# Performance work log

Hardware: AMD Instinct MI355X
Metric: run time of the kernel (lower is better)

Reference implementation:

```python
import jax, jax.numpy as jnp
import numpy as np

B, S, V = 1, 4096, 50265
D, H, DH, FF, L = 768, 12, 64, 3072, 12
W = 256  # one-sided window (longformer-base attention_window=512)
EPS = 1e-5
NEG = -1e9


def _ln(x, s, b):
    mu = jnp.mean(x, -1, keepdims=True)
    var = jnp.mean(jnp.square(x - mu), -1, keepdims=True)
    return (x - mu) * jax.lax.rsqrt(var + EPS) * s + b


def _sliding_attn(q, k, v, key_mask):
    # q,k,v: [B,H,S,DH]; key_mask: [B,S] (1 = attend). Banded attention |i-j| <= W.
    b, h, s, dh = q.shape
    c = W
    nc = s // c
    idx = jnp.arange(nc)[:, None] * c + jnp.arange(3 * c)[None, :]  # index into padded key axis
    kp = jnp.pad(k, ((0, 0), (0, 0), (c, c), (0, 0)))
    vp = jnp.pad(v, ((0, 0), (0, 0), (c, c), (0, 0)))
    k3 = kp[:, :, idx]  # [B,H,nc,3c,DH]
    v3 = vp[:, :, idx]
    qc = q.reshape(b, h, nc, c, dh)
    scores = jnp.einsum('bhncd,bhnmd->bhncm', qc, k3) * (1.0 / (dh ** 0.5))
    rel = jnp.arange(3 * c)[None, :] - c - jnp.arange(c)[:, None]  # key_pos - query_pos, [c,3c]
    band = jnp.abs(rel) <= W
    km = jnp.pad(key_mask.astype(bool), ((0, 0), (c, c)))[:, idx]  # [B,nc,3c]
    valid = band[None, None, None] & km[:, None, :, None, :]
    probs = jax.nn.softmax(jnp.where(valid, scores, NEG), axis=-1)
    out = jnp.einsum('bhncm,bhnmd->bhncd', probs, v3)
    return out.reshape(b, h, s, dh)


def _forward(input_ids, attention_mask, word_emb, pos_emb, emb_ln_s, emb_ln_b,
             Wq, bq, Wk, bk, Wv, bv, Wo, bo, ln1_s, ln1_b,
             W1, b1, W2, b2, ln2_s, ln2_b,
             h1w, h1b, h2w, h2b, h3w, h3b):
    b, s = input_ids.shape
    pos = jnp.arange(s) + 2  # roberta-style position offset (padding_idx=1)
    x = word_emb[input_ids] + pos_emb[pos][None]
    x = _ln(x, emb_ln_s, emb_ln_b)
    key_mask = attention_mask

    def block(xc, p):
        wq, bq_, wk, bk_, wv, bv_, wo, bo_, l1s, l1b, w1, b1_, w2, b2_, l2s, l2b = p
        q = (xc @ wq + bq_).reshape(b, s, H, DH).transpose(0, 2, 1, 3)
        k = (xc @ wk + bk_).reshape(b, s, H, DH).transpose(0, 2, 1, 3)
        v = (xc @ wv + bv_).reshape(b, s, H, DH).transpose(0, 2, 1, 3)
        a = _sliding_attn(q, k, v, key_mask).transpose(0, 2, 1, 3).reshape(b, s, D)
        xc = _ln(xc + a @ wo + bo_, l1s, l1b)
        hdd = jax.nn.gelu(xc @ w1 + b1_, approximate=False)
        xc = _ln(xc + hdd @ w2 + b2_, l2s, l2b)
        return xc, None

    x, _ = jax.lax.scan(block, x, (Wq, bq, Wk, bk, Wv, bv, Wo, bo,
                                   ln1_s, ln1_b, W1, b1, W2, b2, ln2_s, ln2_b))

    # gather hidden state at last occurrence of token id 2 (</s>) per row
    eq = (input_ids == 2).astype(jnp.int32)
    sep = s - 1 - jnp.argmax(eq[:, ::-1], axis=1)
    emb = x[jnp.arange(b), sep]  # [B, D]

    z = jax.nn.relu(emb @ h1w + h1b)
    z = jax.nn.relu(z @ h2w + h2b)
    return jnp.tanh(z @ h3w + h3b)  # [B, 1]


def setup_inputs() -> dict:
    key = jax.random.key(0)
    ks = jax.random.split(key, 24)
    sc = 0.02

    def n(k, shape):
        return jax.random.normal(k, shape, jnp.float32) * sc

    input_ids = jax.random.randint(ks[0], (B, S), 0, V)
    input_ids = input_ids.at[:, -1].set(2)  # guarantee a </s> token (id 2)
    attention_mask = jnp.ones((B, S), jnp.int32)
    return {
        'input_ids': input_ids,
        'attention_mask': attention_mask,
        'word_emb': n(ks[1], (V, D)),
        'pos_emb': n(ks[2], (S + 2, D)),
        'emb_ln_s': jnp.ones((D,), jnp.float32),
        'emb_ln_b': jnp.zeros((D,), jnp.float32),
        'Wq': n(ks[3], (L, D, D)), 'bq': jnp.zeros((L, D), jnp.float32),
        'Wk': n(ks[4], (L, D, D)), 'bk': jnp.zeros((L, D), jnp.float32),
        'Wv': n(ks[5], (L, D, D)), 'bv': jnp.zeros((L, D), jnp.float32),
        'Wo': n(ks[6], (L, D, D)), 'bo': jnp.zeros((L, D), jnp.float32),
        'ln1_s': jnp.ones((L, D), jnp.float32), 'ln1_b': jnp.zeros((L, D), jnp.float32),
        'W1': n(ks[7], (L, D, FF)), 'b1': jnp.zeros((L, FF), jnp.float32),
        'W2': n(ks[8], (L, FF, D)), 'b2': jnp.zeros((L, D), jnp.float32),
        'ln2_s': jnp.ones((L, D), jnp.float32), 'ln2_b': jnp.zeros((L, D), jnp.float32),
        'h1w': n(ks[9], (D, 512)), 'h1b': jnp.zeros((512,), jnp.float32),
        'h2w': n(ks[10], (512, 256)), 'h2b': jnp.zeros((256,), jnp.float32),
        'h3w': n(ks[11], (256, 1)), 'h3b': jnp.zeros((1,), jnp.float32),
    }


def reference(input_ids, attention_mask, word_emb, pos_emb, emb_ln_s, emb_ln_b,
              Wq, bq, Wk, bk, Wv, bv, Wo, bo, ln1_s, ln1_b,
              W1, b1, W2, b2, ln2_s, ln2_b,
              h1w, h1b, h2w, h2b, h3w, h3b):
    return _forward(input_ids, attention_mask, word_emb, pos_emb, emb_ln_s, emb_ln_b,
                    Wq, bq, Wk, bk, Wv, bv, Wo, bo, ln1_s, ln1_b,
                    W1, b1, W2, b2, ln2_s, ln2_b,
                    h1w, h1b, h2w, h2b, h3w, h3b)
```

## Files before the change

kernel.cpp:

```cpp
#include <hip/hip_runtime.h>
#include <math.h>

#define S_LEN 4096
#define DMODEL 768
#define NHEAD 12
#define DHEAD 64
#define FFDIM 3072
#define NLAYER 12
#define WIN 256
#define QKVN 2304

typedef __bf16 bf16x8 __attribute__((ext_vector_type(8)));
typedef unsigned short u16x8 __attribute__((ext_vector_type(8)));
typedef float f32x4 __attribute__((ext_vector_type(4)));

__device__ inline unsigned short f2bf(float f) {
    unsigned int u = __float_as_uint(f);
    u += 0x7fff + ((u >> 16) & 1);
    return (unsigned short)(u >> 16);
}

__device__ inline void gload16(const void* g, void* l) {
    __builtin_amdgcn_global_load_lds((const __attribute__((address_space(1))) void*)g,
                                     (__attribute__((address_space(3))) void*)l, 16, 0, 0);
}


__device__ inline void block_reduce2(float& sum, float& sq) {
    #pragma unroll
    for (int off = 32; off; off >>= 1) {
        sum += __shfl_xor(sum, off);
        sq  += __shfl_xor(sq, off);
    }
    __shared__ float red[8];
    int wid = threadIdx.x >> 6, lane = threadIdx.x & 63;
    if (lane == 0) { red[wid] = sum; red[wid + 4] = sq; }
    __syncthreads();
    sum = red[0] + red[1] + red[2] + red[3];
    sq  = red[4] + red[5] + red[6] + red[7];
    __syncthreads();
}

__global__ __launch_bounds__(256) void ln_kernel(const float* __restrict__ in,
                                                 const float* __restrict__ s,
                                                 const float* __restrict__ b,
                                                 float* __restrict__ out,
                                                 unsigned short* __restrict__ outb) {
    int row = blockIdx.x, tid = threadIdx.x;
    const float* p = in + (size_t)row * DMODEL;
    float v0 = p[tid], v1 = p[tid + 256], v2 = p[tid + 512];
    float sum = v0 + v1 + v2;
    float sq  = v0 * v0 + v1 * v1 + v2 * v2;
    block_reduce2(sum, sq);
    float mu = sum * (1.0f / DMODEL);
    float var = sq * (1.0f / DMODEL) - mu * mu;
    float rs = rsqrtf(var + 1e-5f);
    float* o = out + (size_t)row * DMODEL;
    unsigned short* ob = outb + (size_t)row * DMODEL;
    float r0 = (v0 - mu) * rs * s[tid]       + b[tid];
    float r1 = (v1 - mu) * rs * s[tid + 256] + b[tid + 256];
    float r2 = (v2 - mu) * rs * s[tid + 512] + b[tid + 512];
    o[tid] = r0; o[tid + 256] = r1; o[tid + 512] = r2;
    ob[tid] = f2bf(r0); ob[tid + 256] = f2bf(r1); ob[tid + 512] = f2bf(r2);
}

__global__ __launch_bounds__(256) void embed_ln_kernel(const int* __restrict__ ids,
                                                       const float* __restrict__ wemb,
                                                       const float* __restrict__ pemb,
                                                       const float* __restrict__ s,
                                                       const float* __restrict__ b,
                                                       float* __restrict__ out,
                                                       unsigned short* __restrict__ outb) {
    int row = blockIdx.x, tid = threadIdx.x;
    int id = ids[row];
    const float* wp = wemb + (size_t)id * DMODEL;
    const float* pp = pemb + (size_t)(row + 2) * DMODEL;
    float v0 = wp[tid] + pp[tid];
    float v1 = wp[tid + 256] + pp[tid + 256];
    float v2 = wp[tid + 512] + pp[tid + 512];
    float sum = v0 + v1 + v2;
    float sq  = v0 * v0 + v1 * v1 + v2 * v2;
    block_reduce2(sum, sq);
    float mu = sum * (1.0f / DMODEL);
    float var = sq * (1.0f / DMODEL) - mu * mu;
    float rs = rsqrtf(var + 1e-5f);
    float* o = out + (size_t)row * DMODEL;
    unsigned short* ob = outb + (size_t)row * DMODEL;
    float r0 = (v0 - mu) * rs * s[tid]       + b[tid];
    float r1 = (v1 - mu) * rs * s[tid + 256] + b[tid + 256];
    float r2 = (v2 - mu) * rs * s[tid + 512] + b[tid + 512];
    o[tid] = r0; o[tid + 256] = r1; o[tid + 512] = r2;
    ob[tid] = f2bf(r0); ob[tid + 256] = f2bf(r1); ob[tid + 512] = f2bf(r2);
}

__global__ __launch_bounds__(256) void transpose_all(const float* __restrict__ wq,
                                                     const float* __restrict__ wk,
                                                     const float* __restrict__ wv,
                                                     const float* __restrict__ wo,
                                                     const float* __restrict__ w1,
                                                     const float* __restrict__ w2,
                                                     unsigned short* __restrict__ dq,
                                                     unsigned short* __restrict__ dk,
                                                     unsigned short* __restrict__ dv,
                                                     unsigned short* __restrict__ dwo,
                                                     unsigned short* __restrict__ d1,
                                                     unsigned short* __restrict__ d2) {
    const int id = blockIdx.x;
    const float* src; unsigned short* dst; int C, R, bx, by;
    if (id < 2304) {
        const int m = id / 576, t2 = id % 576;
        src = (m == 0) ? wq : (m == 1) ? wk : (m == 2) ? wv : wo;
        dst = (m == 0) ? dq : (m == 1) ? dk : (m == 2) ? dv : dwo;
        R = 768; C = 768; bx = (t2 % 24) * 32; by = (t2 / 24) * 32;
    } else if (id < 4608) {
        const int t2 = id - 2304;
        src = w1; dst = d1; R = 768; C = 3072;
        bx = (t2 % 96) * 32; by = (t2 / 96) * 32;
    } else {
        const int t2 = id - 4608;
        src = w2; dst = d2; R = 3072; C = 768;
        bx = (t2 % 24) * 32; by = (t2 / 24) * 32;
    }
    __shared__ float tile[32][33];
    const int tx = threadIdx.x & 31, ty = threadIdx.x >> 5;
    #pragma unroll
    for (int k = 0; k < 4; ++k)
        tile[ty + k * 8][tx] = src[(size_t)(by + ty + k * 8) * C + bx + tx];
    __syncthreads();
    #pragma unroll
    for (int k = 0; k < 4; ++k)
        dst[(size_t)(bx + ty + k * 8) * R + by + tx] = f2bf(tile[tx][ty + k * 8]);
}

__global__ __launch_bounds__(256) void bias_concat(const float* __restrict__ bq,
                                                   const float* __restrict__ bk,
                                                   const float* __restrict__ bv,
                                                   float* __restrict__ out) {
    int l = blockIdx.x, t = threadIdx.x;
    for (int i = t; i < DMODEL; i += 256) {
        out[(size_t)l * QKVN + i]              = bq[(size_t)l * DMODEL + i];
        out[(size_t)l * QKVN + DMODEL + i]     = bk[(size_t)l * DMODEL + i];
        out[(size_t)l * QKVN + 2 * DMODEL + i] = bv[(size_t)l * DMODEL + i];
    }
}

template<int MODE, int BN>
__global__ __launch_bounds__(256) void mfma_gemm(const unsigned short* __restrict__ A,
                                                 const unsigned short* __restrict__ Bt,
                                                 const float* __restrict__ bias,
                                                 const float* __restrict__ res,
                                                 void* __restrict__ Cout,
                                                 int M, int N, int K) {
    constexpr int MR = (BN == 128) ? 4 : 2;
    __shared__ unsigned short As[128 * 64];
    __shared__ unsigned short Bs[BN * 64];
    const int tid = threadIdx.x;
    const int wv = tid >> 6, lane = tid & 63;
    const int bm = blockIdx.x * 128, bn = blockIdx.y * BN;
    const int wr = (BN == 128) ? (wv >> 1) * 64 : wv * 32;
    const int wc = (BN == 128) ? (wv & 1) * 64 : 0;
    const int l15 = lane & 15, g = lane >> 4;

    f32x4 acc[MR][4];
    #pragma unroll
    for (int m = 0; m < MR; ++m)
        #pragma unroll
        for (int n = 0; n < 4; ++n)
            #pragma unroll
            for (int e = 0; e < 4; ++e) acc[m][n][e] = 0.f;

    const int srow = tid >> 3;
    const int scol = (tid & 7) * 8;

    for (int k0 = 0; k0 < K; k0 += 64) {
        __syncthreads();
        #pragma unroll
        for (int c = 0; c < 4; ++c)
            gload16(A + (size_t)(bm + c * 32 + srow) * K + k0 + scol,
                    (char*)As + c * 4096 + wv * 1024);
        #pragma unroll
        for (int c = 0; c < BN / 32; ++c)
            gload16(Bt + (size_t)(bn + c * 32 + srow) * K + k0 + scol,
                    (char*)Bs + c * 4096 + wv * 1024);
        __syncthreads();
        #pragma unroll
        for (int kk = 0; kk < 2; ++kk) {
            bf16x8 af[MR], bfr[4];
            #pragma unroll
            for (int m = 0; m < MR; ++m)
                af[m] = *(const bf16x8*)(As + (wr + m * 16 + l15) * 64 + kk * 32 + g * 8);
            #pragma unroll
            for (int n = 0; n < 4; ++n)
                bfr[n] = *(const bf16x8*)(Bs + (wc + n * 16 + l15) * 64 + kk * 32 + g * 8);
            #pragma unroll
            for (int m = 0; m < MR; ++m)
                #pragma unroll
                for (int n = 0; n < 4; ++n)
                    acc[m][n] = __builtin_amdgcn_mfma_f32_16x16x32_bf16(af[m], bfr[n], acc[m][n], 0, 0, 0);
        }
    }

    #pragma unroll
    for (int m = 0; m < MR; ++m) {
        const int row0 = bm + wr + m * 16 + g * 4;
        #pragma unroll
        for (int n = 0; n < 4; ++n) {
            const int col = bn + wc + n * 16 + l15;
            const float bb = bias[col];
            #pragma unroll
            for (int r = 0; r < 4; ++r) {
                float v = acc[m][n][r] + bb;
                if (MODE == 0) {
                    v += res[(size_t)(row0 + r) * N + col];
                    ((float*)Cout)[(size_t)(row0 + r) * N + col] = v;
                } else if (MODE == 1) {
                    ((unsigned short*)Cout)[(size_t)(row0 + r) * N + col] = f2bf(v);
                } else {
                    float gv = 0.5f * v * (1.0f + erff(v * 0.70710678118654752f));
                    ((unsigned short*)Cout)[(size_t)(row0 + r) * N + col] = f2bf(gv);
                }
            }
        }
    }
}

__global__ __launch_bounds__(256) void attn_mfma(const unsigned short* __restrict__ qkv,
                                                 const int* __restrict__ msk,
                                                 unsigned short* __restrict__ aout) {
    __shared__ unsigned short Ks[64 * 64];
    __shared__ unsigned short Vt[64 * 64];
    __shared__ unsigned short Ps[4][16 * 64];
    const int tid = threadIdx.x;
    const int wv = tid >> 6, lane = tid & 63;
    const int l15 = lane & 15, g = lane >> 4;
    const int h = blockIdx.y;
    const int q0 = blockIdx.x * 64;

    const int qrow = q0 + wv * 16 + l15;
    bf16x8 qf[2];
    #pragma unroll
    for (int kk = 0; kk < 2; ++kk)
        qf[kk] = *(const bf16x8*)(qkv + (size_t)qrow * QKVN + h * 64 + kk * 32 + g * 8);

    f32x4 o[4];
    #pragma unroll
    for (int n = 0; n < 4; ++n)
        #pragma unroll
        for (int e = 0; e < 4; ++e) o[n][e] = 0.f;
    float mst[4] = {-3e38f, -3e38f, -3e38f, -3e38f};
    float lst[4] = {0.f, 0.f, 0.f, 0.f};

    const int srow = tid >> 3;
    const int scol = (tid & 7) * 8;
    const int xr  = (l15 & 7) << 3;

    for (int c = 0; c < 9; ++c) {
        const int kc = q0 - 256 + c * 64;
        __syncthreads();
        #pragma unroll
        for (int cc = 0; cc < 2; ++cc) {
            const int r = cc * 32 + srow;
            int krow = min(max(kc + r, 0), S_LEN - 1);
            gload16(qkv + (size_t)krow * QKVN + DMODEL + h * 64 + (scol ^ ((r & 7) << 3)),
                    (char*)Ks + cc * 4096 + wv * 1024);
        }
        #pragma unroll
        for (int cc = 0; cc < 2; ++cc) {
            const int r = cc * 32 + srow;
            int vrow = min(max(kc + r, 0), S_LEN - 1);
            u16x8 vvv = *(const u16x8*)(qkv + (size_t)vrow * QKVN + 2 * DMODEL + h * 64 + scol);
            const int xb = (scol >> 3) & 7;
            #pragma unroll
            for (int j = 0; j < 8; ++j)
                Vt[(scol + j) * 64 + (r ^ ((xb ^ j) << 3))] = vvv[j];
        }
        __syncthreads();

        f32x4 s[4];
        #pragma unroll
        for (int n = 0; n < 4; ++n)
            #pragma unroll
            for (int e = 0; e < 4; ++e) s[n][e] = 0.f;
        #pragma unroll
        for (int kk = 0; kk < 2; ++kk) {
            #pragma unroll
            for (int n = 0; n < 4; ++n) {
                bf16x8 kf = *(const bf16x8*)(Ks + (n * 16 + l15) * 64 + ((kk * 32 + g * 8) ^ xr));
                s[n] = __builtin_amdgcn_mfma_f32_16x16x32_bf16(qf[kk], kf, s[n], 0, 0, 0);
            }
        }

        float pv[4][4];
        const int qbase = q0 + wv * 16 + g * 4;
        #pragma unroll
        for (int n = 0; n < 4; ++n) {
            const int key = kc + n * 16 + l15;
            const bool kin = (key >= 0) && (key < S_LEN);
            const int mv = kin ? msk[key] : 0;
            #pragma unroll
            for (int r = 0; r < 4; ++r) {
                const int qa = qbase + r;
                const bool valid = (mv != 0) && (abs(key - qa) <= WIN);
                pv[n][r] = valid ? s[n][r] * 0.125f : -1e9f;
            }
        }
        float scold[4];
        #pragma unroll
        for (int r = 0; r < 4; ++r) {
            float mx = fmaxf(fmaxf(pv[0][r], pv[1][r]), fmaxf(pv[2][r], pv[3][r]));
            mx = fmaxf(mx, __shfl_xor(mx, 1));
            mx = fmaxf(mx, __shfl_xor(mx, 2));
            mx = fmaxf(mx, __shfl_xor(mx, 4));
            mx = fmaxf(mx, __shfl_xor(mx, 8));
            const float nm = fmaxf(mst[r], mx);
            scold[r] = expf(mst[r] - nm);
            float sum = 0.f;
            #pragma unroll
            for (int n = 0; n < 4; ++n) { pv[n][r] = expf(pv[n][r] - nm); sum += pv[n][r]; }
            sum += __shfl_xor(sum, 1); sum += __shfl_xor(sum, 2);
            sum += __shfl_xor(sum, 4); sum += __shfl_xor(sum, 8);
            lst[r] = lst[r] * scold[r] + sum;
            mst[r] = nm;
        }
        #pragma unroll
        for (int n = 0; n < 4; ++n)
            #pragma unroll
            for (int r = 0; r < 4; ++r)
                o[n][r] *= scold[r];

        #pragma unroll
        for (int n = 0; n < 4; ++n)
            #pragma unroll
            for (int r = 0; r < 4; ++r) {
                const int ql = g * 4 + r;
                Ps[wv][ql * 64 + ((n * 16 + l15) ^ ((ql & 7) << 3))] = f2bf(pv[n][r]);
            }

        #pragma unroll
        for (int kk = 0; kk < 2; ++kk) {
            bf16x8 pf = *(const bf16x8*)(Ps[wv] + l15 * 64 + ((kk * 32 + g * 8) ^ xr));
            #pragma unroll
            for (int nd = 0; nd < 4; ++nd) {
                const int d = nd * 16 + l15;
                const int xv = (((nd * 2 + (l15 >> 3)) & 7) ^ (l15 & 7)) << 3;
                bf16x8 vf = *(const bf16x8*)(Vt + d * 64 + ((kk * 32 + g * 8) ^ xv));
                o[nd] = __builtin_amdgcn_mfma_f32_16x16x32_bf16(pf, vf, o[nd], 0, 0, 0);
            }
        }
    }

    #pragma unroll
    for (int r = 0; r < 4; ++r) {
        const float inv = 1.0f / lst[r];
        const int qa = q0 + wv * 16 + g * 4 + r;
        #pragma unroll
        for (int nd = 0; nd < 4; ++nd)
            aout[(size_t)qa * DMODEL + h * 64 + nd * 16 + l15] = f2bf(o[nd][r] * inv);
    }
}

__global__ __launch_bounds__(256) void head1_kernel(const int* __restrict__ ids,
                                                    const float* __restrict__ x,
                                                    const float* __restrict__ w1,
                                                    const float* __restrict__ b1,
                                                    float* __restrict__ z1) {
    const int tid = threadIdx.x;
    __shared__ int sred[256];
    int loc = -1;
    for (int i = tid; i < S_LEN; i += 256)
        if (ids[i] == 2) loc = i;
    sred[tid] = loc;
    __syncthreads();
    for (int s2 = 128; s2; s2 >>= 1) {
        if (tid < s2) sred[tid] = max(sred[tid], sred[tid + s2]);
        __syncthreads();
    }
    const int sep = sred[0] < 0 ? (S_LEN - 1) : sred[0];

    __shared__ float emb[DMODEL];
    for (int d = tid; d < DMODEL; d += 256) emb[d] = x[(size_t)sep * DMODEL + d];
    __syncthreads();

    const int o = blockIdx.x * 64 + (tid & 63);
    const int chunk = tid >> 6;
    float s = 0.f;
    const int d0 = chunk * 192;
    for (int d = d0; d < d0 + 192; ++d)
        s += emb[d] * w1[(size_t)d * 512 + o];
    __shared__ float part[4][64];
    part[chunk][tid & 63] = s;
    __syncthreads();
    if (chunk == 0) {
        float v = part[0][tid] + part[1][tid] + part[2][tid] + part[3][tid] + b1[o];
        z1[o] = fmaxf(v, 0.f);
    }
}

__global__ __launch_bounds__(256) void head2_kernel(const float* __restrict__ z1,
                                                    const float* __restrict__ w2,
                                                    const float* __restrict__ b2,
                                                    const float* __restrict__ w3,
                                                    const float* __restrict__ b3,
                                                    float* __restrict__ out) {
    const int tid = threadIdx.x;
    __shared__ float z1s[512];
    for (int i = tid; i < 512; i += 256) z1s[i] = z1[i];
    __syncthreads();
    float s = b2[tid];
    for (int d = 0; d < 512; ++d) s += z1s[d] * w2[(size_t)d * 256 + tid];
    float z2 = fmaxf(s, 0.f);
    __shared__ float fred[256];
    fred[tid] = z2 * w3[tid];
    __syncthreads();
    for (int s2 = 128; s2; s2 >>= 1) {
        if (tid < s2) fred[tid] += fred[tid + s2];
        __syncthreads();
    }
    if (tid == 0) out[0] = tanhf(fred[0] + b3[0]);
}


extern "C" void kernel_launch(void* const* d_in, const int* in_sizes, int n_in,
                              void* d_out, int out_size, void* d_ws, size_t ws_size,
                              hipStream_t stream) {
    const int*   ids      = (const int*)d_in[0];
    const int*   amask    = (const int*)d_in[1];
    const float* word_emb = (const float*)d_in[2];
    const float* pos_emb  = (const float*)d_in[3];
    const float* emb_s    = (const float*)d_in[4];
    const float* emb_b    = (const float*)d_in[5];
    const float* Wq = (const float*)d_in[6];
    const float* bq = (const float*)d_in[7];
    const float* Wk = (const float*)d_in[8];
    const float* bk = (const float*)d_in[9];
    const float* Wv = (const float*)d_in[10];
    const float* bv = (const float*)d_in[11];
    const float* Wo = (const float*)d_in[12];
    const float* bo = (const float*)d_in[13];
    const float* l1s = (const float*)d_in[14];
    const float* l1b = (const float*)d_in[15];
    const float* W1 = (const float*)d_in[16];
    const float* b1 = (const float*)d_in[17];
    const float* W2 = (const float*)d_in[18];
    const float* b2 = (const float*)d_in[19];
    const float* l2s = (const float*)d_in[20];
    const float* l2b = (const float*)d_in[21];
    const float* h1w = (const float*)d_in[22];
    const float* h1b = (const float*)d_in[23];
    const float* h2w = (const float*)d_in[24];
    const float* h2b = (const float*)d_in[25];
    const float* h3w = (const float*)d_in[26];
    const float* h3b = (const float*)d_in[27];

    char* ws = (char*)d_ws;
    float* x          = (float*)(ws);
    float* t          = (float*)(ws + 12582912);
    unsigned short* xb   = (unsigned short*)(ws + 25165824);
    unsigned short* qkv  = (unsigned short*)(ws + 31457280);
    unsigned short* a    = (unsigned short*)(ws + 50331648);
    unsigned short* hb   = (unsigned short*)(ws + 56623104);
    unsigned short* WqkvT= (unsigned short*)(ws + 81788928);
    unsigned short* WoT  = (unsigned short*)(ws + 85327872);
    unsigned short* W1T  = (unsigned short*)(ws + 86507520);
    unsigned short* W2T  = (unsigned short*)(ws + 91226112);
    float* biascat       = (float*)(ws + 95944704);
    float* z1ws          = (float*)(ws + 96055296);

    bias_concat<<<NLAYER, 256, 0, stream>>>(bq, bk, bv, biascat);
    embed_ln_kernel<<<S_LEN, 256, 0, stream>>>(ids, word_emb, pos_emb, emb_s, emb_b, x, xb);

    const size_t dd = (size_t)DMODEL * DMODEL;
    const size_t df = (size_t)DMODEL * FFDIM;

    for (int l = 0; l < NLAYER; ++l) {
        transpose_all<<<6912, 256, 0, stream>>>(Wq + l * dd, Wk + l * dd, Wv + l * dd, Wo + l * dd,
                                                W1 + l * df, W2 + l * df,
                                                WqkvT, WqkvT + dd, WqkvT + 2 * dd, WoT, W1T, W2T);

        mfma_gemm<1, 128><<<dim3(32, 18), 256, 0, stream>>>(xb, WqkvT, biascat + (size_t)l * QKVN,
                                                            nullptr, qkv, S_LEN, QKVN, DMODEL);
        attn_mfma<<<dim3(S_LEN / 64, NHEAD), 256, 0, stream>>>(qkv, amask, a);

        mfma_gemm<0, 64><<<dim3(32, 12), 256, 0, stream>>>(a, WoT, bo + (size_t)l * DMODEL,
                                                           x, t, S_LEN, DMODEL, DMODEL);
        ln_kernel<<<S_LEN, 256, 0, stream>>>(t, l1s + (size_t)l * DMODEL, l1b + (size_t)l * DMODEL, x, xb);

        mfma_gemm<2, 128><<<dim3(32, 24), 256, 0, stream>>>(xb, W1T, b1 + (size_t)l * FFDIM,
                                                            nullptr, hb, S_LEN, FFDIM, DMODEL);
        mfma_gemm<0, 64><<<dim3(32, 12), 256, 0, stream>>>(hb, W2T, b2 + (size_t)l * DMODEL,
                                                           x, t, S_LEN, DMODEL, FFDIM);
        ln_kernel<<<S_LEN, 256, 0, stream>>>(t, l2s + (size_t)l * DMODEL, l2b + (size_t)l * DMODEL, x, xb);
    }

    head1_kernel<<<8, 256, 0, stream>>>(ids, x, h1w, h1b, z1ws);
    head2_kernel<<<1, 256, 0, stream>>>(z1ws, h2w, h2b, h3w, h3b, (float*)d_out);
}
```

Before: 2.747 ms.

## Batch all-layer weight transposes into one launch and widen attention query tile

The per-layer weight transpose/convert kernels are replaced by a single launch that converts all twelve layers' weights into a contiguous bf16 buffer before the layer loop. This cuts launch count and lets the conversion run as one large grid. The attention kernel now gives each wave 32 query rows instead of 16, so each K/V chunk loaded into shared memory serves twice as many queries. The cost is ten key chunks instead of nine, more registers per thread and half as many blocks, which lowers parallelism. The workspace grows to hold every layer's converted weights.

```diff
diff --git a/kernel.cpp b/kernel.cpp
--- a/kernel.cpp
+++ b/kernel.cpp
@@ -13,6 +13,10 @@
 typedef __bf16 bf16x8 __attribute__((ext_vector_type(8)));
 typedef unsigned short u16x8 __attribute__((ext_vector_type(8)));
 typedef float f32x4 __attribute__((ext_vector_type(4)));
+
+#define WDD 589824
+#define WDF 2359296
+#define WLAYER 7077888
 
 __device__ inline unsigned short f2bf(float f) {
     unsigned int u = __float_as_uint(f);
@@ -93,33 +97,30 @@
     ob[tid] = f2bf(r0); ob[tid + 256] = f2bf(r1); ob[tid + 512] = f2bf(r2);
 }
 
-__global__ __launch_bounds__(256) void transpose_all(const float* __restrict__ wq,
-                                                     const float* __restrict__ wk,
-                                                     const float* __restrict__ wv,
-                                                     const float* __restrict__ wo,
-                                                     const float* __restrict__ w1,
-                                                     const float* __restrict__ w2,
-                                                     unsigned short* __restrict__ dq,
-                                                     unsigned short* __restrict__ dk,
-                                                     unsigned short* __restrict__ dv,
-                                                     unsigned short* __restrict__ dwo,
-                                                     unsigned short* __restrict__ d1,
-                                                     unsigned short* __restrict__ d2) {
-    const int id = blockIdx.x;
+__global__ __launch_bounds__(256) void transpose_all(const float* __restrict__ Wq,
+                                                     const float* __restrict__ Wk,
+                                                     const float* __restrict__ Wv,
+                                                     const float* __restrict__ Wo,
+                                                     const float* __restrict__ W1,
+                                                     const float* __restrict__ W2,
+                                                     unsigned short* __restrict__ wall) {
+    const int l  = blockIdx.x / 6912;
+    const int id = blockIdx.x % 6912;
+    unsigned short* base = wall + (size_t)l * WLAYER;
     const float* src; unsigned short* dst; int C, R, bx, by;
     if (id < 2304) {
         const int m = id / 576, t2 = id % 576;
-        src = (m == 0) ? wq : (m == 1) ? wk : (m == 2) ? wv : wo;
-        dst = (m == 0) ? dq : (m == 1) ? dk : (m == 2) ? dv : dwo;
+        src = ((m == 0) ? Wq : (m == 1) ? Wk : (m == 2) ? Wv : Wo) + (size_t)l * WDD;
+        dst = base + (size_t)m * WDD;
         R = 768; C = 768; bx = (t2 % 24) * 32; by = (t2 / 24) * 32;
     } else if (id < 4608) {
         const int t2 = id - 2304;
-        src = w1; dst = d1; R = 768; C = 3072;
-        bx = (t2 % 96) * 32; by = (t2 / 96) * 32;
+        src = W1 + (size_t)l * WDF; dst = base + 4 * (size_t)WDD;
+        R = 768; C = 3072; bx = (t2 % 96) * 32; by = (t2 / 96) * 32;
     } else {
         const int t2 = id - 4608;
-        src = w2; dst = d2; R = 3072; C = 768;
-        bx = (t2 % 24) * 32; by = (t2 / 24) * 32;
+        src = W2 + (size_t)l * WDF; dst = base + 4 * (size_t)WDD + WDF;
+        R = 3072; C = 768; bx = (t2 % 24) * 32; by = (t2 / 24) * 32;
     }
     __shared__ float tile[32][33];
     const int tx = threadIdx.x & 31, ty = threadIdx.x >> 5;
@@ -229,32 +230,40 @@
                                                  unsigned short* __restrict__ aout) {
     __shared__ unsigned short Ks[64 * 64];
     __shared__ unsigned short Vt[64 * 64];
-    __shared__ unsigned short Ps[4][16 * 64];
+    __shared__ unsigned short Ps[4][32 * 64];
     const int tid = threadIdx.x;
     const int wv = tid >> 6, lane = tid & 63;
     const int l15 = lane & 15, g = lane >> 4;
     const int h = blockIdx.y;
-    const int q0 = blockIdx.x * 64;
-
-    const int qrow = q0 + wv * 16 + l15;
-    bf16x8 qf[2];
-    #pragma unroll
-    for (int kk = 0; kk < 2; ++kk)
-        qf[kk] = *(const bf16x8*)(qkv + (size_t)qrow * QKVN + h * 64 + kk * 32 + g * 8);
-
-    f32x4 o[4];
-    #pragma unroll
-    for (int n = 0; n < 4; ++n)
-        #pragma unroll
-        for (int e = 0; e < 4; ++e) o[n][e] = 0.f;
-    float mst[4] = {-3e38f, -3e38f, -3e38f, -3e38f};
-    float lst[4] = {0.f, 0.f, 0.f, 0.f};
+    const int q0 = blockIdx.x * 128;
+
+    bf16x8 qf[2][2];
+    #pragma unroll
+    for (int m = 0; m < 2; ++m) {
+        const int qrow = q0 + wv * 32 + m * 16 + l15;
+        #pragma unroll
+        for (int kk = 0; kk < 2; ++kk)
+            qf[m][kk] = *(const bf16x8*)(qkv + (size_t)qrow * QKVN + h * 64 + kk * 32 + g * 8);
+    }
+
+    f32x4 o[2][4];
+    #pragma unroll
+    for (int m = 0; m < 2; ++m)
+        #pragma unroll
+        for (int n = 0; n < 4; ++n)
+            #pragma unroll
+            for (int e = 0; e < 4; ++e) o[m][n][e] = 0.f;
+    float mst[2][4], lst[2][4];
+    #pragma unroll
+    for (int m = 0; m < 2; ++m)
+        #pragma unroll
+        for (int r = 0; r < 4; ++r) { mst[m][r] = -3e38f; lst[m][r] = 0.f; }
 
     const int srow = tid >> 3;
     const int scol = (tid & 7) * 8;
     const int xr  = (l15 & 7) << 3;
 
-    for (int c = 0; c < 9; ++c) {
+    for (int c = 0; c < 10; ++c) {
         const int kc = q0 - 256 + c * 64;
         __syncthreads();
         #pragma unroll
@@ -276,87 +285,104 @@
         }
         __syncthreads();
 
-        f32x4 s[4];
-        #pragma unroll
-        for (int n = 0; n < 4; ++n)
-            #pragma unroll
-            for (int e = 0; e < 4; ++e) s[n][e] = 0.f;
+        f32x4 s[2][4];
+        #pragma unroll
+        for (int m = 0; m < 2; ++m)
+            #pragma unroll
+            for (int n = 0; n < 4; ++n)
+                #pragma unroll
+                for (int e = 0; e < 4; ++e) s[m][n][e] = 0.f;
         #pragma unroll
         for (int kk = 0; kk < 2; ++kk) {
+            bf16x8 kf[4];
+            #pragma unroll
+            for (int n = 0; n < 4; ++n)
+                kf[n] = *(const bf16x8*)(Ks + (n * 16 + l15) * 64 + ((kk * 32 + g * 8) ^ xr));
+            #pragma unroll
+            for (int m = 0; m < 2; ++m)
+                #pragma unroll
+                for (int n = 0; n < 4; ++n)
+                    s[m][n] = __builtin_amdgcn_mfma_f32_16x16x32_bf16(qf[m][kk], kf[n], s[m][n], 0, 0, 0);
+        }
+
+        #pragma unroll
+        for (int m = 0; m < 2; ++m) {
+            float pv[4][4];
+            const int qbase = q0 + wv * 32 + m * 16 + g * 4;
             #pragma unroll
             for (int n = 0; n < 4; ++n) {
-                bf16x8 kf = *(const bf16x8*)(Ks + (n * 16 + l15) * 64 + ((kk * 32 + g * 8) ^ xr));
-                s[n] = __builtin_amdgcn_mfma_f32_16x16x32_bf16(qf[kk], kf, s[n], 0, 0, 0);
+                const int key = kc + n * 16 + l15;
+                const bool kin = (key >= 0) && (key < S_LEN);
+                const int mv = kin ? msk[key] : 0;
+                #pragma unroll
+                for (int r = 0; r < 4; ++r) {
+                    const int qa = qbase + r;
+                    const bool valid = (mv != 0) && (abs(key - qa) <= WIN);
+                    pv[n][r] = valid ? s[m][n][r] * 0.125f : -1e9f;
+                }
             }
-        }
-
-        float pv[4][4];
-        const int qbase = q0 + wv * 16 + g * 4;
-        #pragma unroll
-        for (int n = 0; n < 4; ++n) {
-            const int key = kc + n * 16 + l15;
-            const bool kin = (key >= 0) && (key < S_LEN);
-            const int mv = kin ? msk[key] : 0;
+            float scold[4];
             #pragma unroll
             for (int r = 0; r < 4; ++r) {
-                const int qa = qbase + r;
-                const bool valid = (mv != 0) && (abs(key - qa) <= WIN);
-                pv[n][r] = valid ? s[n][r] * 0.125f : -1e9f;
+                float mx = fmaxf(fmaxf(pv[0][r], pv[1][r]), fmaxf(pv[2][r], pv[3][r]));
+                mx = fmaxf(mx, __shfl_xor(mx, 1));
+                mx = fmaxf(mx, __shfl_xor(mx, 2));
+                mx = fmaxf(mx, __shfl_xor(mx, 4));
+                mx = fmaxf(mx, __shfl_xor(mx, 8));
+                const float nm = fmaxf(mst[m][r], mx);
+                scold[r] = expf(mst[m][r] - nm);
+                float sum = 0.f;
+                #pragma unroll
+                for (int n = 0; n < 4; ++n) { pv[n][r] = expf(pv[n][r] - nm); sum += pv[n][r]; }
+                sum += __shfl_xor(sum, 1); sum += __shfl_xor(sum, 2);
+                sum += __shfl_xor(sum, 4); sum += __shfl_xor(sum, 8);
+                lst[m][r] = lst[m][r] * scold[r] + sum;
+                mst[m][r] = nm;
             }
-        }
-        float scold[4];
-        #pragma unroll
-        for (int r = 0; r < 4; ++r) {
-            float mx = fmaxf(fmaxf(pv[0][r], pv[1][r]), fmaxf(pv[2][r], pv[3][r]));
-            mx = fmaxf(mx, __shfl_xor(mx, 1));
-            mx = fmaxf(mx, __shfl_xor(mx, 2));
-            mx = fmaxf(mx, __shfl_xor(mx, 4));
-            mx = fmaxf(mx, __shfl_xor(mx, 8));
-            const float nm = fmaxf(mst[r], mx);
-            scold[r] = expf(mst[r] - nm);
-            float sum = 0.f;
-            #pragma unroll
-            for (int n = 0; n < 4; ++n) { pv[n][r] = expf(pv[n][r] - nm); sum += pv[n][r]; }
-            sum += __shfl_xor(sum, 1); sum += __shfl_xor(sum, 2);
-            sum += __shfl_xor(sum, 4); sum += __shfl_xor(sum, 8);
-            lst[r] = lst[r] * scold[r] + sum;
-            mst[r] = nm;
-        }
-        #pragma unroll
-        for (int n = 0; n < 4; ++n)
-            #pragma unroll
-            for (int r = 0; r < 4; ++r)
-                o[n][r] *= scold[r];
-
-        #pragma unroll
-        for (int n = 0; n < 4; ++n)
-            #pragma unroll
-            for (int r = 0; r < 4; ++r) {
-                const int ql = g * 4 + r;
-                Ps[wv][ql * 64 + ((n * 16 + l15) ^ ((ql & 7) << 3))] = f2bf(pv[n][r]);
-            }
+            #pragma unroll
+            for (int n = 0; n < 4; ++n)
+                #pragma unroll
+                for (int r = 0; r < 4; ++r)
+                    o[m][n][r] *= scold[r];
+
+            #pragma unroll
+            for (int n = 0; n < 4; ++n)
+                #pragma unroll
+                for (int r = 0; r < 4; ++r) {
+                    const int ql = m * 16 + g * 4 + r;
+                    Ps[wv][ql * 64 + ((n * 16 + l15) ^ ((ql & 7) << 3))] = f2bf(pv[n][r]);
+                }
+        }
 
         #pragma unroll
         for (int kk = 0; kk < 2; ++kk) {
-            bf16x8 pf = *(const bf16x8*)(Ps[wv] + l15 * 64 + ((kk * 32 + g * 8) ^ xr));
+            bf16x8 vf[4];
             #pragma unroll
             for (int nd = 0; nd < 4; ++nd) {
                 const int d = nd * 16 + l15;
                 const int xv = (((nd * 2 + (l15 >> 3)) & 7) ^ (l15 & 7)) << 3;
-                bf16x8 vf = *(const bf16x8*)(Vt + d * 64 + ((kk * 32 + g * 8) ^ xv));
-                o[nd] = __builtin_amdgcn_mfma_f32_16x16x32_bf16(pf, vf, o[nd], 0, 0, 0);
+                vf[nd] = *(const bf16x8*)(Vt + d * 64 + ((kk * 32 + g * 8) ^ xv));
             }
-        }
-    }
-
-    #pragma unroll
-    for (int r = 0; r < 4; ++r) {
-        const float inv = 1.0f / lst[r];
-        const int qa = q0 + wv * 16 + g * 4 + r;
-        #pragma unroll
-        for (int nd = 0; nd < 4; ++nd)
-            aout[(size_t)qa * DMODEL + h * 64 + nd * 16 + l15] = f2bf(o[nd][r] * inv);
-    }
+            #pragma unroll
+            for (int m = 0; m < 2; ++m) {
+                bf16x8 pf = *(const bf16x8*)(Ps[wv] + (m * 16 + l15) * 64 + ((kk * 32 + g * 8) ^ xr));
+                #pragma unroll
+                for (int nd = 0; nd < 4; ++nd)
+                    o[m][nd] = __builtin_amdgcn_mfma_f32_16x16x32_bf16(pf, vf[nd], o[m][nd], 0, 0, 0);
+            }
+        }
+    }
+
+    #pragma unroll
+    for (int m = 0; m < 2; ++m)
+        #pragma unroll
+        for (int r = 0; r < 4; ++r) {
+            const float inv = 1.0f / lst[m][r];
+            const int qa = q0 + wv * 32 + m * 16 + g * 4 + r;
+            #pragma unroll
+            for (int nd = 0; nd < 4; ++nd)
+                aout[(size_t)qa * DMODEL + h * 64 + nd * 16 + l15] = f2bf(o[m][nd][r] * inv);
+        }
 }
 
 __global__ __launch_bounds__(256) void head1_kernel(const int* __restrict__ ids,
@@ -459,27 +485,23 @@
     unsigned short* qkv  = (unsigned short*)(ws + 31457280);
     unsigned short* a    = (unsigned short*)(ws + 50331648);
     unsigned short* hb   = (unsigned short*)(ws + 56623104);
-    unsigned short* WqkvT= (unsigned short*)(ws + 81788928);
-    unsigned short* WoT  = (unsigned short*)(ws + 85327872);
-    unsigned short* W1T  = (unsigned short*)(ws + 86507520);
-    unsigned short* W2T  = (unsigned short*)(ws + 91226112);
-    float* biascat       = (float*)(ws + 95944704);
-    float* z1ws          = (float*)(ws + 96055296);
+    float* biascat       = (float*)(ws + 81788928);
+    float* z1ws          = (float*)(ws + 81920000);
+    unsigned short* wall = (unsigned short*)(ws + 100663296);
 
     bias_concat<<<NLAYER, 256, 0, stream>>>(bq, bk, bv, biascat);
+    transpose_all<<<6912 * NLAYER, 256, 0, stream>>>(Wq, Wk, Wv, Wo, W1, W2, wall);
     embed_ln_kernel<<<S_LEN, 256, 0, stream>>>(ids, word_emb, pos_emb, emb_s, emb_b, x, xb);
 
-    const size_t dd = (size_t)DMODEL * DMODEL;
-    const size_t df = (size_t)DMODEL * FFDIM;
-
     for (int l = 0; l < NLAYER; ++l) {
-        transpose_all<<<6912, 256, 0, stream>>>(Wq + l * dd, Wk + l * dd, Wv + l * dd, Wo + l * dd,
-                                                W1 + l * df, W2 + l * df,
-                                                WqkvT, WqkvT + dd, WqkvT + 2 * dd, WoT, W1T, W2T);
+        const unsigned short* WqkvT = wall + (size_t)l * WLAYER;
+        const unsigned short* WoT   = WqkvT + 3 * (size_t)WDD;
+        const unsigned short* W1T   = WqkvT + 4 * (size_t)WDD;
+        const unsigned short* W2T   = WqkvT + 4 * (size_t)WDD + WDF;
 
         mfma_gemm<1, 128><<<dim3(32, 18), 256, 0, stream>>>(xb, WqkvT, biascat + (size_t)l * QKVN,
                                                             nullptr, qkv, S_LEN, QKVN, DMODEL);
-        attn_mfma<<<dim3(S_LEN / 64, NHEAD), 256, 0, stream>>>(qkv, amask, a);
+        attn_mfma<<<dim3(S_LEN / 128, NHEAD), 256, 0, stream>>>(qkv, amask, a);
 
         mfma_gemm<0, 64><<<dim3(32, 12), 256, 0, stream>>>(a, WoT, bo + (size_t)l * DMODEL,
                                                            x, t, S_LEN, DMODEL, DMODEL);
```

New measurement: 3.288 ms. 1.2x slower.

## Batch all-layer weight transposes into one launch, vectorize stores, templatize GEMM dims

Applied to the files above, without the earlier changes.

Replaces the twelve per-layer transpose launches with a single launch that converts every layer's weights into a persistent per-layer bf16 buffer before the layer loop. The transpose write path now packs two bf16 values into 32-bit stores, and the GEMM problem sizes become template parameters so the compiler sees them as constants. The goal is to cut launch count and serialization between the transpose and the GEMMs, and to make both the transposes and the GEMM loops cheaper. In exchange it needs a much larger workspace holding all transposed layers, and that buffer must fit within the allocated workspace.

```diff
diff --git a/kernel.cpp b/kernel.cpp
--- a/kernel.cpp
+++ b/kernel.cpp
@@ -13,6 +13,10 @@
 typedef __bf16 bf16x8 __attribute__((ext_vector_type(8)));
 typedef unsigned short u16x8 __attribute__((ext_vector_type(8)));
 typedef float f32x4 __attribute__((ext_vector_type(4)));
+
+#define WDD 589824
+#define WDF 2359296
+#define WLAYER 7077888
 
 __device__ inline unsigned short f2bf(float f) {
     unsigned int u = __float_as_uint(f);
@@ -93,33 +97,30 @@
     ob[tid] = f2bf(r0); ob[tid + 256] = f2bf(r1); ob[tid + 512] = f2bf(r2);
 }
 
-__global__ __launch_bounds__(256) void transpose_all(const float* __restrict__ wq,
-                                                     const float* __restrict__ wk,
-                                                     const float* __restrict__ wv,
-                                                     const float* __restrict__ wo,
-                                                     const float* __restrict__ w1,
-                                                     const float* __restrict__ w2,
-                                                     unsigned short* __restrict__ dq,
-                                                     unsigned short* __restrict__ dk,
-                                                     unsigned short* __restrict__ dv,
-                                                     unsigned short* __restrict__ dwo,
-                                                     unsigned short* __restrict__ d1,
-                                                     unsigned short* __restrict__ d2) {
-    const int id = blockIdx.x;
+__global__ __launch_bounds__(256) void transpose_all(const float* __restrict__ Wq,
+                                                     const float* __restrict__ Wk,
+                                                     const float* __restrict__ Wv,
+                                                     const float* __restrict__ Wo,
+                                                     const float* __restrict__ W1,
+                                                     const float* __restrict__ W2,
+                                                     unsigned short* __restrict__ wall) {
+    const int l  = blockIdx.x / 6912;
+    const int id = blockIdx.x % 6912;
+    unsigned short* base = wall + (size_t)l * WLAYER;
     const float* src; unsigned short* dst; int C, R, bx, by;
     if (id < 2304) {
         const int m = id / 576, t2 = id % 576;
-        src = (m == 0) ? wq : (m == 1) ? wk : (m == 2) ? wv : wo;
-        dst = (m == 0) ? dq : (m == 1) ? dk : (m == 2) ? dv : dwo;
+        src = ((m == 0) ? Wq : (m == 1) ? Wk : (m == 2) ? Wv : Wo) + (size_t)l * WDD;
+        dst = base + (size_t)m * WDD;
         R = 768; C = 768; bx = (t2 % 24) * 32; by = (t2 / 24) * 32;
     } else if (id < 4608) {
         const int t2 = id - 2304;
-        src = w1; dst = d1; R = 768; C = 3072;
-        bx = (t2 % 96) * 32; by = (t2 / 96) * 32;
+        src = W1 + (size_t)l * WDF; dst = base + 4 * (size_t)WDD;
+        R = 768; C = 3072; bx = (t2 % 96) * 32; by = (t2 / 96) * 32;
     } else {
         const int t2 = id - 4608;
-        src = w2; dst = d2; R = 3072; C = 768;
-        bx = (t2 % 24) * 32; by = (t2 / 24) * 32;
+        src = W2 + (size_t)l * WDF; dst = base + 4 * (size_t)WDD + WDF;
+        R = 3072; C = 768; bx = (t2 % 24) * 32; by = (t2 / 24) * 32;
     }
     __shared__ float tile[32][33];
     const int tx = threadIdx.x & 31, ty = threadIdx.x >> 5;
@@ -127,9 +128,15 @@
     for (int k = 0; k < 4; ++k)
         tile[ty + k * 8][tx] = src[(size_t)(by + ty + k * 8) * C + bx + tx];
     __syncthreads();
-    #pragma unroll
-    for (int k = 0; k < 4; ++k)
-        dst[(size_t)(bx + ty + k * 8) * R + by + tx] = f2bf(tile[tx][ty + k * 8]);
+    const int c16 = threadIdx.x >> 4;
+    const int rp  = threadIdx.x & 15;
+    #pragma unroll
+    for (int k = 0; k < 2; ++k) {
+        const int c = c16 + k * 16;
+        unsigned int lo = f2bf(tile[2 * rp][c]);
+        unsigned int hi = f2bf(tile[2 * rp + 1][c]);
+        *(unsigned int*)&dst[(size_t)(bx + c) * R + by + 2 * rp] = (hi << 16) | lo;
+    }
 }
 
 __global__ __launch_bounds__(256) void bias_concat(const float* __restrict__ bq,
@@ -144,13 +151,12 @@
     }
 }
 
-template<int MODE, int BN>
+template<int MODE, int BN, int M, int N, int K>
 __global__ __launch_bounds__(256) void mfma_gemm(const unsigned short* __restrict__ A,
                                                  const unsigned short* __restrict__ Bt,
                                                  const float* __restrict__ bias,
                                                  const float* __restrict__ res,
-                                                 void* __restrict__ Cout,
-                                                 int M, int N, int K) {
+                                                 void* __restrict__ Cout) {
     constexpr int MR = (BN == 128) ? 4 : 2;
     __shared__ unsigned short As[128 * 64];
     __shared__ unsigned short Bs[BN * 64];
@@ -459,36 +465,32 @@
     unsigned short* qkv  = (unsigned short*)(ws + 31457280);
     unsigned short* a    = (unsigned short*)(ws + 50331648);
     unsigned short* hb   = (unsigned short*)(ws + 56623104);
-    unsigned short* WqkvT= (unsigned short*)(ws + 81788928);
-    unsigned short* WoT  = (unsigned short*)(ws + 85327872);
-    unsigned short* W1T  = (unsigned short*)(ws + 86507520);
-    unsigned short* W2T  = (unsigned short*)(ws + 91226112);
-    float* biascat       = (float*)(ws + 95944704);
-    float* z1ws          = (float*)(ws + 96055296);
+    float* biascat       = (float*)(ws + 81788928);
+    float* z1ws          = (float*)(ws + 81920000);
+    unsigned short* wall = (unsigned short*)(ws + 100663296);
 
     bias_concat<<<NLAYER, 256, 0, stream>>>(bq, bk, bv, biascat);
+    transpose_all<<<6912 * NLAYER, 256, 0, stream>>>(Wq, Wk, Wv, Wo, W1, W2, wall);
     embed_ln_kernel<<<S_LEN, 256, 0, stream>>>(ids, word_emb, pos_emb, emb_s, emb_b, x, xb);
 
-    const size_t dd = (size_t)DMODEL * DMODEL;
-    const size_t df = (size_t)DMODEL * FFDIM;
-
     for (int l = 0; l < NLAYER; ++l) {
-        transpose_all<<<6912, 256, 0, stream>>>(Wq + l * dd, Wk + l * dd, Wv + l * dd, Wo + l * dd,
-                                                W1 + l * df, W2 + l * df,
-                                                WqkvT, WqkvT + dd, WqkvT + 2 * dd, WoT, W1T, W2T);
-
-        mfma_gemm<1, 128><<<dim3(32, 18), 256, 0, stream>>>(xb, WqkvT, biascat + (size_t)l * QKVN,
-                                                            nullptr, qkv, S_LEN, QKVN, DMODEL);
+        const unsigned short* WqkvT = wall + (size_t)l * WLAYER;
+        const unsigned short* WoT   = WqkvT + 3 * (size_t)WDD;
+        const unsigned short* W1T   = WqkvT + 4 * (size_t)WDD;
+        const unsigned short* W2T   = WqkvT + 4 * (size_t)WDD + WDF;
+
+        mfma_gemm<1, 128, S_LEN, QKVN, DMODEL><<<dim3(32, 18), 256, 0, stream>>>(
+            xb, WqkvT, biascat + (size_t)l * QKVN, nullptr, qkv);
         attn_mfma<<<dim3(S_LEN / 64, NHEAD), 256, 0, stream>>>(qkv, amask, a);
 
-        mfma_gemm<0, 64><<<dim3(32, 12), 256, 0, stream>>>(a, WoT, bo + (size_t)l * DMODEL,
-                                                           x, t, S_LEN, DMODEL, DMODEL);
+        mfma_gemm<0, 64, S_LEN, DMODEL, DMODEL><<<dim3(32, 12), 256, 0, stream>>>(
+            a, WoT, bo + (size_t)l * DMODEL, x, t);
         ln_kernel<<<S_LEN, 256, 0, stream>>>(t, l1s + (size_t)l * DMODEL, l1b + (size_t)l * DMODEL, x, xb);
 
-        mfma_gemm<2, 128><<<dim3(32, 24), 256, 0, stream>>>(xb, W1T, b1 + (size_t)l * FFDIM,
-                                                            nullptr, hb, S_LEN, FFDIM, DMODEL);
-        mfma_gemm<0, 64><<<dim3(32, 12), 256, 0, stream>>>(hb, W2T, b2 + (size_t)l * DMODEL,
-                                                           x, t, S_LEN, DMODEL, FFDIM);
+        mfma_gemm<2, 128, S_LEN, FFDIM, DMODEL><<<dim3(32, 24), 256, 0, stream>>>(
+            xb, W1T, b1 + (size_t)l * FFDIM, nullptr, hb);
+        mfma_gemm<0, 64, S_LEN, DMODEL, FFDIM><<<dim3(32, 12), 256, 0, stream>>>(
+            hb, W2T, b2 + (size_t)l * DMODEL, x, t);
         ln_kernel<<<S_LEN, 256, 0, stream>>>(t, l2s + (size_t)l * DMODEL, l2b + (size_t)l * DMODEL, x, xb);
     }
 
```

New measurement: 2.999 ms. 1.09x slower.

## Double-buffer K/V tiles in sliding attention and vectorize weight transpose

Applied to the files above, without the earlier changes.

The attention kernel now keeps two LDS buffers for K and V. While the current 64-key chunk is being computed, the next chunk is loaded into the other buffer, so global-load latency overlaps with MFMA work and one barrier per iteration is removed. Separately, the fp32-to-bf16 weight transpose kernel now reads with float4 loads and writes packed 4-element uint2 stores. The cost is doubled K/V LDS footprint, which may reduce occupancy, and the V transpose store into the next buffer happens while other waves are still reading the current one.

```diff
diff --git a/kernel.cpp b/kernel.cpp
--- a/kernel.cpp
+++ b/kernel.cpp
@@ -122,14 +122,25 @@
         bx = (t2 % 24) * 32; by = (t2 / 24) * 32;
     }
     __shared__ float tile[32][33];
-    const int tx = threadIdx.x & 31, ty = threadIdx.x >> 5;
-    #pragma unroll
-    for (int k = 0; k < 4; ++k)
-        tile[ty + k * 8][tx] = src[(size_t)(by + ty + k * 8) * C + bx + tx];
-    __syncthreads();
-    #pragma unroll
-    for (int k = 0; k < 4; ++k)
-        dst[(size_t)(bx + ty + k * 8) * R + by + tx] = f2bf(tile[tx][ty + k * 8]);
+    const int t = threadIdx.x;
+    const int lrow = t >> 3;
+    const int lcol = (t & 7) * 4;
+    float4 v = *(const float4*)&src[(size_t)(by + lrow) * C + bx + lcol];
+    tile[lrow][lcol]     = v.x;
+    tile[lrow][lcol + 1] = v.y;
+    tile[lrow][lcol + 2] = v.z;
+    tile[lrow][lcol + 3] = v.w;
+    __syncthreads();
+    const int c  = t >> 3;
+    const int rp = t & 7;
+    unsigned int b0 = f2bf(tile[4 * rp][c]);
+    unsigned int b1 = f2bf(tile[4 * rp + 1][c]);
+    unsigned int b2 = f2bf(tile[4 * rp + 2][c]);
+    unsigned int b3 = f2bf(tile[4 * rp + 3][c]);
+    uint2 pk;
+    pk.x = (b1 << 16) | b0;
+    pk.y = (b3 << 16) | b2;
+    *(uint2*)&dst[(size_t)(bx + c) * R + by + 4 * rp] = pk;
 }
 
 __global__ __launch_bounds__(256) void bias_concat(const float* __restrict__ bq,
@@ -227,8 +238,8 @@
 __global__ __launch_bounds__(256) void attn_mfma(const unsigned short* __restrict__ qkv,
                                                  const int* __restrict__ msk,
                                                  unsigned short* __restrict__ aout) {
-    __shared__ unsigned short Ks[64 * 64];
-    __shared__ unsigned short Vt[64 * 64];
+    __shared__ unsigned short Ks[2][64 * 64];
+    __shared__ unsigned short Vt[2][64 * 64];
     __shared__ unsigned short Ps[4][16 * 64];
     const int tid = threadIdx.x;
     const int wv = tid >> 6, lane = tid & 63;
@@ -253,28 +264,52 @@
     const int srow = tid >> 3;
     const int scol = (tid & 7) * 8;
     const int xr  = (l15 & 7) << 3;
-
-    for (int c = 0; c < 9; ++c) {
-        const int kc = q0 - 256 + c * 64;
-        __syncthreads();
+    const int xb  = (scol >> 3) & 7;
+
+    {
+        const int kc = q0 - 256;
         #pragma unroll
         for (int cc = 0; cc < 2; ++cc) {
             const int r = cc * 32 + srow;
             int krow = min(max(kc + r, 0), S_LEN - 1);
             gload16(qkv + (size_t)krow * QKVN + DMODEL + h * 64 + (scol ^ ((r & 7) << 3)),
-                    (char*)Ks + cc * 4096 + wv * 1024);
+                    (char*)Ks[0] + cc * 4096 + wv * 1024);
         }
         #pragma unroll
         for (int cc = 0; cc < 2; ++cc) {
             const int r = cc * 32 + srow;
             int vrow = min(max(kc + r, 0), S_LEN - 1);
             u16x8 vvv = *(const u16x8*)(qkv + (size_t)vrow * QKVN + 2 * DMODEL + h * 64 + scol);
-            const int xb = (scol >> 3) & 7;
             #pragma unroll
             for (int j = 0; j < 8; ++j)
-                Vt[(scol + j) * 64 + (r ^ ((xb ^ j) << 3))] = vvv[j];
+                Vt[0][(scol + j) * 64 + (r ^ ((xb ^ j) << 3))] = vvv[j];
         }
         __syncthreads();
+    }
+
+    for (int c = 0; c < 9; ++c) {
+        const int cur = c & 1, nxt = cur ^ 1;
+        const int kc = q0 - 256 + c * 64;
+
+        if (c < 8) {
+            const int kcn = kc + 64;
+            #pragma unroll
+            for (int cc = 0; cc < 2; ++cc) {
+                const int r = cc * 32 + srow;
+                int krow = min(max(kcn + r, 0), S_LEN - 1);
+                gload16(qkv + (size_t)krow * QKVN + DMODEL + h * 64 + (scol ^ ((r & 7) << 3)),
+                        (char*)Ks[nxt] + cc * 4096 + wv * 1024);
+            }
+            #pragma unroll
+            for (int cc = 0; cc < 2; ++cc) {
+                const int r = cc * 32 + srow;
+                int vrow = min(max(kcn + r, 0), S_LEN - 1);
+                u16x8 vvv = *(const u16x8*)(qkv + (size_t)vrow * QKVN + 2 * DMODEL + h * 64 + scol);
+                #pragma unroll
+                for (int j = 0; j < 8; ++j)
+                    Vt[nxt][(scol + j) * 64 + (r ^ ((xb ^ j) << 3))] = vvv[j];
+            }
+        }
 
         f32x4 s[4];
         #pragma unroll
@@ -285,7 +320,7 @@
         for (int kk = 0; kk < 2; ++kk) {
             #pragma unroll
             for (int n = 0; n < 4; ++n) {
-                bf16x8 kf = *(const bf16x8*)(Ks + (n * 16 + l15) * 64 + ((kk * 32 + g * 8) ^ xr));
+                bf16x8 kf = *(const bf16x8*)(Ks[cur] + (n * 16 + l15) * 64 + ((kk * 32 + g * 8) ^ xr));
                 s[n] = __builtin_amdgcn_mfma_f32_16x16x32_bf16(qf[kk], kf, s[n], 0, 0, 0);
             }
         }
@@ -343,10 +378,12 @@
             for (int nd = 0; nd < 4; ++nd) {
                 const int d = nd * 16 + l15;
                 const int xv = (((nd * 2 + (l15 >> 3)) & 7) ^ (l15 & 7)) << 3;
-                bf16x8 vf = *(const bf16x8*)(Vt + d * 64 + ((kk * 32 + g * 8) ^ xv));
+                bf16x8 vf = *(const bf16x8*)(Vt[cur] + d * 64 + ((kk * 32 + g * 8) ^ xv));
                 o[nd] = __builtin_amdgcn_mfma_f32_16x16x32_bf16(pf, vf, o[nd], 0, 0, 0);
             }
         }
+
+        __syncthreads();
     }
 
     #pragma unroll
```

After: 2.774 ms. No clear change (+1.0%).
